# Performance work log

Hardware: AMD Instinct MI355X
Metric: run time of the kernel (lower is better)

The kernel has to match this reference:

```python
import jax, jax.numpy as jnp
from jax import lax
import numpy as np

B, T, F = 256, 2048, 12
EV_VOCAB, RS_VOCAB = 32, 8
EED, RED = 6, 3
H, K = 96, 3
D = F + EED + RED  # 21


def setup_inputs() -> dict:
    key = jax.random.key(0)
    ks = jax.random.split(key, 12)
    s = 0.05
    return {
        'seq': jax.random.normal(ks[0], (B, T, F), jnp.float32),
        'ev': jax.random.randint(ks[1], (B, T), 0, EV_VOCAB),
        'rs': jax.random.randint(ks[2], (B, T), 0, RS_VOCAB),
        'lengths': jax.random.randint(ks[3], (B,), 1, T + 1),  # valid lengths in [1, T]
        'event_emb': jax.random.normal(ks[4], (EV_VOCAB, EED), jnp.float32) * s,
        'result_emb': jax.random.normal(ks[5], (RS_VOCAB, RED), jnp.float32) * s,
        'W_ih': jax.random.normal(ks[6], (4 * H, D), jnp.float32) * s,
        'W_hh': jax.random.normal(ks[7], (4 * H, H), jnp.float32) * s,
        'b_ih': jnp.zeros((4 * H,), jnp.float32),
        'b_hh': jnp.zeros((4 * H,), jnp.float32),
        'W_mlp': jax.random.normal(ks[8], (H, H * K), jnp.float32) * s,
        'b_mlp': jnp.zeros((H,), jnp.float32),
        'W_fc': jax.random.normal(ks[9], (2, 2 * H), jnp.float32) * s,
        'b_fc': jnp.zeros((2,), jnp.float32),
    }


def reference(seq, ev, rs, lengths, event_emb, result_emb, W_ih, W_hh, b_ih, b_hh,
              W_mlp, b_mlp, W_fc, b_fc):
    # embed + concat -> [B,T,D]
    x = jnp.concatenate([seq, event_emb[ev], result_emb[rs]], axis=-1)
    xs = jnp.swapaxes(x, 0, 1)  # [T,B,D]
    ts = jnp.arange(T)
    b = b_ih + b_hh

    def step(carry, inp):
        h, c = carry
        x_t, t = inp
        gates = x_t @ W_ih.T + h @ W_hh.T + b  # [B,4H]
        i, f, g, o = jnp.split(gates, 4, axis=-1)  # PyTorch gate order i,f,g,o
        i = jax.nn.sigmoid(i); f = jax.nn.sigmoid(f)
        g = jnp.tanh(g); o = jax.nn.sigmoid(o)
        c_new = f * c + i * g
        h_new = o * jnp.tanh(c_new)
        m = (t < lengths)[:, None]  # packed-seq semantics: freeze state past length
        h = jnp.where(m, h_new, h)
        c = jnp.where(m, c_new, c)
        out = jnp.where(m, h_new, jnp.zeros_like(h_new))  # pad_packed zeros
        return (h, c), out

    h0 = jnp.zeros((B, H), x.dtype)
    (h_fin, _), outs = lax.scan(step, (h0, h0), (xs, ts))
    out_padded = jnp.swapaxes(outs, 0, 1)  # [B,T,H]

    # vectorized last-k gather (replaces torch Python loop)
    idx = lengths[:, None] - K + jnp.arange(K)  # [B,K]
    valid = idx >= 0
    gathered = jnp.take_along_axis(out_padded, jnp.clip(idx, 0)[:, :, None], axis=1)
    gathered = jnp.where(valid[:, :, None], gathered, jnp.zeros_like(gathered))
    lastk = gathered.reshape(B, K * H)

    h_lastk = jax.nn.relu(lastk @ W_mlp.T + b_mlp)
    h = jnp.concatenate([h_fin, h_lastk], axis=1)  # [B,2H]
    return h @ W_fc.T + b_fc  # [B,2]
```

## Files before the change

### kernel.cpp

```cpp
#include <hip/hip_runtime.h>

#define TT 2048
#define FF 12
#define HH 96
#define CH 128
#define L2E 1.44269504088896340736f

__device__ __forceinline__ float fast_exp2(float x){ return __builtin_amdgcn_exp2f(x); }
__device__ __forceinline__ float fast_rcp(float x){ return __builtin_amdgcn_rcpf(x); }

#define DPPF(x, ctrl) __int_as_float(__builtin_amdgcn_update_dpp(0, __float_as_int(x), (ctrl), 0xF, 0xF, true))
#define QP_XOR1 0xB1
#define QP_XOR2 0x4E
#define SHL4    0x104
#define SHL8    0x108
#define SHL12   0x10C

__global__ __launch_bounds__(512, 2) void lstm_persist(
  const float* __restrict__ seq, const int* __restrict__ ev, const int* __restrict__ rsi,
  const int* __restrict__ len, const float* __restrict__ eemb, const float* __restrict__ remb,
  const float* __restrict__ W_ih, const float* __restrict__ W_hh,
  const float* __restrict__ b_ih, const float* __restrict__ b_hh,
  const float* __restrict__ W_mlp, const float* __restrict__ b_mlp,
  const float* __restrict__ W_fc, const float* __restrict__ b_fc,
  float* __restrict__ out)
{
  const int b   = blockIdx.x;
  const int tid = threadIdx.x;
  const int G   = tid >> 4;
  const int lu  = tid & 15;
  const int q   = lu >> 2;
  const int c4  = lu & 3;

  __shared__ __align__(16) float vv[2][128];
  __shared__ __align__(16) float xch[CH][32];
  __shared__ __align__(16) float lastk[3*HH];
  __shared__ __align__(16) float et[32*6];
  __shared__ __align__(16) float rt[8*3];
  __shared__ __align__(16) float accs[192];
  __shared__ __align__(16) float h2[2*HH];
  __shared__ int evb[CH];
  __shared__ int rsb[CH];

  float wh[3][24];
  float wx[3][6];
  float bg[3];
  bool  isT[3];
  #pragma unroll
  for (int j = 0; j < 3; ++j) {
    const int rp = 12*G + 3*q + j;
    const int u_ = rp >> 2;
    const int qg = rp & 3;
    const int grow = qg*96 + u_;
    const float* ph = W_hh + grow*96 + 24*c4;
    #pragma unroll
    for (int i = 0; i < 24; ++i) wh[j][i] = ph[i];
    #pragma unroll
    for (int i = 0; i < 6; ++i) {
      const int cc = 6*c4 + i;
      wx[j][i] = (cc < 21) ? W_ih[grow*21 + cc] : 0.f;
    }
    bg[j]  = (c4 == 0) ? (b_ih[grow] + b_hh[grow]) : 0.f;
    isT[j] = (qg == 2);
  }
  const int un = 3*G + lu;

  if (tid < 256) ((float*)vv)[tid] = 0.f;
  for (int i = tid; i < 3*HH; i += 512) lastk[i] = 0.f;
  for (int i = tid; i < 192;  i += 512) et[i] = eemb[i];
  for (int i = tid; i < 24;   i += 512) rt[i] = remb[i];

  float c_state = 0.f;
  const int L = len[b];

  for (int t0 = 0; t0 < L; t0 += CH) {
    for (int i = tid; i < CH*FF; i += 512) {
      const int r = i / 12;
      const int c = i - r*12;
      xch[r][c] = seq[(size_t)b*(TT*FF) + (size_t)t0*FF + i];
    }
    if (tid < CH) {
      evb[tid] = ev [b*TT + t0 + tid];
      rsb[tid] = rsi[b*TT + t0 + tid];
    }
    __syncthreads();
    for (int i = tid; i < CH*20; i += 512) {
      const int r  = i / 20;
      const int cc = i - r*20 + 12;
      float val;
      if (cc < 18)      val = et[evb[r]*6 + (cc-12)];
      else if (cc < 21) val = rt[rsb[r]*3 + (cc-18)];
      else              val = 0.f;
      xch[r][cc] = val;
    }
    __syncthreads();

    const int nr = min(CH, L - t0);
    for (int r = 0; r < nr; ++r) {
      const int p = (t0 + r) & 1;
      const float* hp = vv[p] + 24*c4;
      float hb[24];
      #pragma unroll
      for (int i = 0; i < 6; ++i) *(float4*)&hb[4*i] = ((const float4*)hp)[i];
      const float* xp = &xch[r][6*c4];
      float xb[6];
      #pragma unroll
      for (int i = 0; i < 3; ++i) *(float2*)&xb[2*i] = ((const float2*)xp)[i];

      float S[3];
      #pragma unroll
      for (int j = 0; j < 3; ++j) {
        float a0 = bg[j], a1 = 0.f, a2 = 0.f;
        #pragma unroll
        for (int i = 0; i < 8; ++i) {
          a0 = fmaf(wh[j][3*i+0], hb[3*i+0], a0);
          a1 = fmaf(wh[j][3*i+1], hb[3*i+1], a1);
          a2 = fmaf(wh[j][3*i+2], hb[3*i+2], a2);
        }
        a0 = fmaf(wx[j][0], xb[0], a0);
        a1 = fmaf(wx[j][1], xb[1], a1);
        a2 = fmaf(wx[j][2], xb[2], a2);
        a0 = fmaf(wx[j][3], xb[3], a0);
        a1 = fmaf(wx[j][4], xb[4], a1);
        a2 = fmaf(wx[j][5], xb[5], a2);
        float s = (a0 + a1) + a2;
        s += DPPF(s, QP_XOR1);
        s += DPPF(s, QP_XOR2);
        S[j] = s;
      }
      float A[3];
      #pragma unroll
      for (int j = 0; j < 3; ++j) {
        const float s = S[j];
        const float arg = isT[j] ? (-2.f*L2E)*fabsf(s) : (-L2E)*s;
        const float e  = fast_exp2(arg);
        const float r1 = fast_rcp(1.f + e);
        A[j] = isT[j] ? copysignf((1.f - e)*r1, s) : r1;
      }
      const float m1 = DPPF(A[0], SHL4);
      const float m2 = DPPF(A[1], SHL4);
      const float m3 = DPPF(A[2], SHL4);
      const float m4 = DPPF(m1,  SHL4);
      const float m5 = DPPF(m2,  SHL4);
      const float s8 = DPPF(A[2], SHL8);
      const float w9 = DPPF(A[0], SHL12);
      const float wa = DPPF(A[1], SHL12);
      const float wb = DPPF(A[2], SHL12);
      if (lu < 3) {
        const float il = (lu==0) ? A[0] : ((lu==1) ? m2 : s8);
        const float fl = (lu==0) ? A[1] : ((lu==1) ? m3 : w9);
        const float gl = (lu==0) ? A[2] : ((lu==1) ? m4 : wa);
        const float ol = (lu==0) ? m1   : ((lu==1) ? m5 : wb);
        c_state = fmaf(fl, c_state, il*gl);
        const float e2 = fast_exp2((-2.f*L2E)*fabsf(c_state));
        const float th = copysignf((1.f - e2)*fast_rcp(1.f + e2), c_state);
        const float hn = ol * th;
        vv[p^1][un] = hn;
        const int kk = (t0 + r) + 3 - L;
        if (kk >= 0) lastk[kk*96 + un] = hn;
      }
      __syncthreads();
    }
  }

  const float* hfin = vv[L & 1];
  if (tid < 192) {
    const int hh = tid / 96;
    const int m  = tid - hh*96;
    const float* wp = W_mlp + m*288 + hh*144;
    const float* xq = lastk + hh*144;
    float s = 0.f;
    #pragma unroll 8
    for (int i = 0; i < 144; ++i) s = fmaf(wp[i], xq[i], s);
    accs[tid] = s;
  }
  __syncthreads();
  if (tid < 96) {
    const float hl = accs[tid] + accs[96+tid] + b_mlp[tid];
    h2[96 + tid] = fmaxf(hl, 0.f);
    h2[tid] = hfin[tid];
  }
  __syncthreads();
  if (tid < 128) {
    const int o  = tid >> 6;
    const int ll = tid & 63;
    const float* wf = W_fc + o*192 + 3*ll;
    float s = fmaf(wf[0], h2[3*ll+0], fmaf(wf[1], h2[3*ll+1], wf[2]*h2[3*ll+2]));
    #pragma unroll
    for (int off = 32; off > 0; off >>= 1) s += __shfl_down(s, off);
    if (ll == 0) out[b*2 + o] = s + b_fc[o];
  }
}

extern "C" void kernel_launch(void* const* d_in, const int* in_sizes, int n_in,
                              void* d_out, int out_size, void* d_ws, size_t ws_size,
                              hipStream_t stream) {
  const float* seq   = (const float*)d_in[0];
  const int*   ev    = (const int*)  d_in[1];
  const int*   rsi   = (const int*)  d_in[2];
  const int*   len   = (const int*)  d_in[3];
  const float* eemb  = (const float*)d_in[4];
  const float* remb  = (const float*)d_in[5];
  const float* W_ih  = (const float*)d_in[6];
  const float* W_hh  = (const float*)d_in[7];
  const float* b_ih  = (const float*)d_in[8];
  const float* b_hh  = (const float*)d_in[9];
  const float* W_mlp = (const float*)d_in[10];
  const float* b_mlp = (const float*)d_in[11];
  const float* W_fc  = (const float*)d_in[12];
  const float* b_fc  = (const float*)d_in[13];

  hipLaunchKernelGGL(lstm_persist, dim3(256), dim3(512), 0, stream,
                     seq, ev, rsi, len, eemb, remb, W_ih, W_hh, b_ih, b_hh,
                     W_mlp, b_mlp, W_fc, b_fc, (float*)d_out);
}
```

Baseline: 1.367 ms.

## Repartition LSTM gate rows to 6 per lane with 8-way column split

Each 16-lane group now handles 3 hidden units, and each lane owns 6 gate rows across 16 concatenated columns (96 h plus 21 x, padded). The h and x buffers are laid out in padded 20-float slices so every lane reads four float4s. The x-projection is folded into the same dot product, and sigmoid and tanh share one exp/rcp formula through per-row constants. This removes the separate x-dot code and most of the gate-gather DPP shuffles. In exchange it adds an extra DPP reduction stage and more registers per lane.

```diff
diff --git a/kernel.cpp b/kernel.cpp
--- a/kernel.cpp
+++ b/kernel.cpp
@@ -4,6 +4,8 @@
 #define FF 12
 #define HH 96
 #define CH 128
+#define SLC 20
+#define XW  40
 #define L2E 1.44269504088896340736f
 
 __device__ __forceinline__ float fast_exp2(float x){ return __builtin_amdgcn_exp2f(x); }
@@ -14,7 +16,6 @@
 #define QP_XOR2 0x4E
 #define SHL4    0x104
 #define SHL8    0x108
-#define SHL12   0x10C
 
 __global__ __launch_bounds__(512, 2) void lstm_persist(
   const float* __restrict__ seq, const int* __restrict__ ev, const int* __restrict__ rsi,
@@ -29,54 +30,53 @@
   const int tid = threadIdx.x;
   const int G   = tid >> 4;
   const int lu  = tid & 15;
-  const int q   = lu >> 2;
-  const int c4  = lu & 3;
+  const int oct = lu >> 3;
+  const int cs  = lu & 7;
 
-  __shared__ __align__(16) float vv[2][128];
-  __shared__ __align__(16) float xch[CH][32];
+  __shared__ __align__(16) float vv[2][8*SLC];
+  __shared__ __align__(16) float xch[CH][XW];
   __shared__ __align__(16) float lastk[3*HH];
-  __shared__ __align__(16) float et[32*6];
-  __shared__ __align__(16) float rt[8*3];
+  __shared__ __align__(16) float et[192];
+  __shared__ __align__(16) float rt[24];
   __shared__ __align__(16) float accs[192];
-  __shared__ __align__(16) float h2[2*HH];
+  __shared__ __align__(16) float h2[192];
   __shared__ int evb[CH];
   __shared__ int rsb[CH];
 
-  float wh[3][24];
-  float wx[3][6];
-  float bg[3];
-  bool  isT[3];
+  float wh[6][16], bg[6], cK[6], cM[6], cB[6];
   #pragma unroll
-  for (int j = 0; j < 3; ++j) {
-    const int rp = 12*G + 3*q + j;
-    const int u_ = rp >> 2;
-    const int qg = rp & 3;
-    const int grow = qg*96 + u_;
-    const float* ph = W_hh + grow*96 + 24*c4;
+  for (int j = 0; j < 6; ++j) {
+    const int lr   = 6*oct + j;
+    const int u_   = 3*G + (lr >> 2);
+    const int gate = lr & 3;
+    const int grow = gate*96 + u_;
     #pragma unroll
-    for (int i = 0; i < 24; ++i) wh[j][i] = ph[i];
-    #pragma unroll
-    for (int i = 0; i < 6; ++i) {
-      const int cc = 6*c4 + i;
-      wx[j][i] = (cc < 21) ? W_ih[grow*21 + cc] : 0.f;
+    for (int i = 0; i < 16; ++i) {
+      const int col = 16*cs + i;
+      wh[j][i] = (col < 96) ? W_hh[grow*96 + col]
+               : ((col < 117) ? W_ih[grow*21 + (col-96)] : 0.f);
     }
-    bg[j]  = (c4 == 0) ? (b_ih[grow] + b_hh[grow]) : 0.f;
-    isT[j] = (qg == 2);
+    bg[j] = (cs == 0) ? (b_ih[grow] + b_hh[grow]) : 0.f;
+    const bool t = (gate == 2);
+    cK[j] = t ? (-2.f*L2E) : (-L2E);
+    cM[j] = t ? 2.f : 1.f;
+    cB[j] = t ? -1.f : 0.f;
   }
-  const int un = 3*G + lu;
+  const int un = 3*G + ((lu == 8) ? 2 : lu);
 
-  if (tid < 256) ((float*)vv)[tid] = 0.f;
-  for (int i = tid; i < 3*HH; i += 512) lastk[i] = 0.f;
-  for (int i = tid; i < 192;  i += 512) et[i] = eemb[i];
-  for (int i = tid; i < 24;   i += 512) rt[i] = remb[i];
+  for (int i = tid; i < 2*8*SLC; i += 512) ((float*)vv)[i]  = 0.f;
+  for (int i = tid; i < CH*XW;   i += 512) ((float*)xch)[i] = 0.f;
+  for (int i = tid; i < 3*HH;    i += 512) lastk[i] = 0.f;
+  if (tid < 192) et[tid] = eemb[tid];
+  if (tid < 24)  rt[tid] = remb[tid];
+  __syncthreads();
 
   float c_state = 0.f;
   const int L = len[b];
 
   for (int t0 = 0; t0 < L; t0 += CH) {
     for (int i = tid; i < CH*FF; i += 512) {
-      const int r = i / 12;
-      const int c = i - r*12;
+      const int r = i / 12, c = i - r*12;
       xch[r][c] = seq[(size_t)b*(TT*FF) + (size_t)t0*FF + i];
     }
     if (tid < CH) {
@@ -84,78 +84,56 @@
       rsb[tid] = rsi[b*TT + t0 + tid];
     }
     __syncthreads();
-    for (int i = tid; i < CH*20; i += 512) {
-      const int r  = i / 20;
-      const int cc = i - r*20 + 12;
-      float val;
-      if (cc < 18)      val = et[evb[r]*6 + (cc-12)];
-      else if (cc < 21) val = rt[rsb[r]*3 + (cc-18)];
-      else              val = 0.f;
-      xch[r][cc] = val;
+    for (int i = tid; i < CH*9; i += 512) {
+      const int r = i / 9, c = 12 + (i - r*9);
+      const float val = (c < 18) ? et[evb[r]*6 + (c-12)] : rt[rsb[r]*3 + (c-18)];
+      xch[r][(c < 16) ? c : (c + 4)] = val;
     }
     __syncthreads();
 
     const int nr = min(CH, L - t0);
     for (int r = 0; r < nr; ++r) {
       const int p = (t0 + r) & 1;
-      const float* hp = vv[p] + 24*c4;
-      float hb[24];
+      const float* vp = (cs < 6) ? (vv[p] + SLC*cs) : (&xch[r][(cs-6)*SLC]);
+      float hb[16];
       #pragma unroll
-      for (int i = 0; i < 6; ++i) *(float4*)&hb[4*i] = ((const float4*)hp)[i];
-      const float* xp = &xch[r][6*c4];
-      float xb[6];
+      for (int i = 0; i < 4; ++i) *(float4*)&hb[4*i] = ((const float4*)vp)[i];
+
+      float S[6];
       #pragma unroll
-      for (int i = 0; i < 3; ++i) *(float2*)&xb[2*i] = ((const float2*)xp)[i];
-
-      float S[3];
-      #pragma unroll
-      for (int j = 0; j < 3; ++j) {
-        float a0 = bg[j], a1 = 0.f, a2 = 0.f;
+      for (int j = 0; j < 6; ++j) {
+        float a0 = bg[j], a1 = 0.f;
         #pragma unroll
         for (int i = 0; i < 8; ++i) {
-          a0 = fmaf(wh[j][3*i+0], hb[3*i+0], a0);
-          a1 = fmaf(wh[j][3*i+1], hb[3*i+1], a1);
-          a2 = fmaf(wh[j][3*i+2], hb[3*i+2], a2);
+          a0 = fmaf(wh[j][2*i],   hb[2*i],   a0);
+          a1 = fmaf(wh[j][2*i+1], hb[2*i+1], a1);
         }
-        a0 = fmaf(wx[j][0], xb[0], a0);
-        a1 = fmaf(wx[j][1], xb[1], a1);
-        a2 = fmaf(wx[j][2], xb[2], a2);
-        a0 = fmaf(wx[j][3], xb[3], a0);
-        a1 = fmaf(wx[j][4], xb[4], a1);
-        a2 = fmaf(wx[j][5], xb[5], a2);
-        float s = (a0 + a1) + a2;
-        s += DPPF(s, QP_XOR1);
-        s += DPPF(s, QP_XOR2);
-        S[j] = s;
+        S[j] = a0 + a1;
       }
-      float A[3];
       #pragma unroll
-      for (int j = 0; j < 3; ++j) {
-        const float s = S[j];
-        const float arg = isT[j] ? (-2.f*L2E)*fabsf(s) : (-L2E)*s;
-        const float e  = fast_exp2(arg);
-        const float r1 = fast_rcp(1.f + e);
-        A[j] = isT[j] ? copysignf((1.f - e)*r1, s) : r1;
+      for (int j = 0; j < 6; ++j) S[j] += DPPF(S[j], SHL4);
+      #pragma unroll
+      for (int j = 0; j < 6; ++j) S[j] += DPPF(S[j], QP_XOR1);
+      #pragma unroll
+      for (int j = 0; j < 6; ++j) S[j] += DPPF(S[j], QP_XOR2);
+      float A[6];
+      #pragma unroll
+      for (int j = 0; j < 6; ++j) {
+        const float e = fast_exp2(cK[j]*S[j]);
+        A[j] = fmaf(cM[j], fast_rcp(1.f + e), cB[j]);
       }
-      const float m1 = DPPF(A[0], SHL4);
-      const float m2 = DPPF(A[1], SHL4);
-      const float m3 = DPPF(A[2], SHL4);
-      const float m4 = DPPF(m1,  SHL4);
-      const float m5 = DPPF(m2,  SHL4);
-      const float s8 = DPPF(A[2], SHL8);
-      const float w9 = DPPF(A[0], SHL12);
-      const float wa = DPPF(A[1], SHL12);
-      const float wb = DPPF(A[2], SHL12);
-      if (lu < 3) {
-        const float il = (lu==0) ? A[0] : ((lu==1) ? m2 : s8);
-        const float fl = (lu==0) ? A[1] : ((lu==1) ? m3 : w9);
-        const float gl = (lu==0) ? A[2] : ((lu==1) ? m4 : wa);
-        const float ol = (lu==0) ? m1   : ((lu==1) ? m5 : wb);
-        c_state = fmaf(fl, c_state, il*gl);
+      const float X0 = DPPF(A[0], SHL8);
+      const float X1 = DPPF(A[1], SHL8);
+      if ((lu == 0) | (lu == 1) | (lu == 8)) {
+        const float i_ = (lu==1) ? A[4] : ((lu==8) ? A[2] : A[0]);
+        const float f_ = (lu==1) ? A[5] : ((lu==8) ? A[3] : A[1]);
+        const float g_ = (lu==1) ? X0   : ((lu==8) ? A[4] : A[2]);
+        const float o_ = (lu==1) ? X1   : ((lu==8) ? A[5] : A[3]);
+        c_state = fmaf(f_, c_state, i_*g_);
         const float e2 = fast_exp2((-2.f*L2E)*fabsf(c_state));
         const float th = copysignf((1.f - e2)*fast_rcp(1.f + e2), c_state);
-        const float hn = ol * th;
-        vv[p^1][un] = hn;
+        const float hn = o_ * th;
+        vv[p^1][SLC*(un >> 4) + (un & 15)] = hn;
         const int kk = (t0 + r) + 3 - L;
         if (kk >= 0) lastk[kk*96 + un] = hn;
       }
@@ -163,7 +141,6 @@
     }
   }
 
-  const float* hfin = vv[L & 1];
   if (tid < 192) {
     const int hh = tid / 96;
     const int m  = tid - hh*96;
@@ -178,7 +155,7 @@
   if (tid < 96) {
     const float hl = accs[tid] + accs[96+tid] + b_mlp[tid];
     h2[96 + tid] = fmaxf(hl, 0.f);
-    h2[tid] = hfin[tid];
+    h2[tid] = vv[L & 1][SLC*(tid >> 4) + (tid & 15)];
   }
   __syncthreads();
   if (tid < 128) {
```

After: 1.455 ms. 1.06x slower.
